# Kernel tuning notes

Hardware: AMD Instinct MI355X
Metric: run time of the kernel (lower is better)

Reference implementation:

```python
import jax, jax.numpy as jnp
import numpy as np

H = 128
L = 3
N = 100000
E = 1600000
G = 1024
OUT = 10
MAX_LEVEL = 1000
MAX_THOUGHTS = 5000
N_CATE = 5
BN_EPS = 1e-5


def _make_pe(n_pos, h):
    pos = np.arange(n_pos, dtype=np.float32)[:, None]
    div = np.exp(np.arange(0, h, 2, dtype=np.float32) * (-np.log(10000.0) / h))
    pe = np.zeros((n_pos, h), dtype=np.float32)
    pe[:, 0::2] = np.sin(pos * div)
    pe[:, 1::2] = np.cos(pos * div)
    return jnp.asarray(pe)


def setup_inputs() -> dict:
    key = jax.random.key(0)
    ks = jax.random.split(key, 16)
    s = 0.02
    inp = {
        "x": jax.random.randint(ks[0], (N, 3), 0, 5, dtype=jnp.int64 if jax.config.jax_enable_x64 else jnp.int32),
        "edge_index": jax.random.randint(ks[1], (2, E), 0, N),
        "batch": jnp.sort(jax.random.randint(ks[2], (N,), 0, G)),
        "num_graphs": G,
        "pe": _make_pe(MAX_THOUGHTS, H),
        "cate_emb": jax.random.normal(ks[3], (N_CATE, H), jnp.float32) * s,
        "level_emb": jax.random.normal(ks[4], (MAX_LEVEL, H), jnp.float32) * s,
        "conv_W1": jax.random.normal(ks[5], (L, H, H), jnp.float32) * s,
        "conv_b1": jnp.zeros((L, H), jnp.float32),
        "conv_g1": jnp.ones((L, H), jnp.float32),
        "conv_be1": jnp.zeros((L, H), jnp.float32),
        "conv_W2": jax.random.normal(ks[6], (L, H, H), jnp.float32) * s,
        "conv_b2": jnp.zeros((L, H), jnp.float32),
        "norm_g": jnp.ones((L, H), jnp.float32),
        "norm_be": jnp.zeros((L, H), jnp.float32),
        "gate_W1": jax.random.normal(ks[7], (H, H), jnp.float32) * s,
        "gate_b1": jnp.zeros((H,), jnp.float32),
        "gate_W2": jax.random.normal(ks[8], (H, 1), jnp.float32) * s,
        "gate_b2": jnp.zeros((1,), jnp.float32),
        "cls_W1": jax.random.normal(ks[9], (H, H), jnp.float32) * s,
        "cls_b1": jnp.zeros((H,), jnp.float32),
        "cls_g": jnp.ones((H,), jnp.float32),
        "cls_be": jnp.zeros((H,), jnp.float32),
        "cls_W2": jax.random.normal(ks[10], (H, OUT), jnp.float32) * s,
        "cls_b2": jnp.zeros((OUT,), jnp.float32),
    }
    return inp


def _bn(h, g, b):
    # BatchNorm1d, training mode: batch stats over the node/graph dim, biased var
    m = jnp.mean(h, axis=0)
    v = jnp.var(h, axis=0)
    return (h - m) * jax.lax.rsqrt(v + BN_EPS) * g + b


def reference(x, edge_index, batch, num_graphs, pe, cate_emb, level_emb,
              conv_W1, conv_b1, conv_g1, conv_be1, conv_W2, conv_b2,
              norm_g, norm_be, gate_W1, gate_b1, gate_W2, gate_b2,
              cls_W1, cls_b1, cls_g, cls_be, cls_W2, cls_b2):
    # NodeEncoder ('tree'): level + cate + sinusoidal thought PE
    level = jnp.clip(x[:, 0], 0, MAX_LEVEL - 1)
    cate = jnp.clip(x[:, 1], 0, N_CATE - 1)
    thought = jnp.clip(x[:, 2], 0, MAX_THOUGHTS - 1)
    h = cate_emb[cate] + level_emb[level] + pe[thought]  # [N, H]

    src, dst = edge_index[0], edge_index[1]
    n = h.shape[0]
    for i in range(L):
        # GINConv (eps=0): h_i <- MLP(h_i + sum_{j->i} h_j)
        agg = jax.ops.segment_sum(h[src], dst, num_segments=n)
        z = (h + agg) @ conv_W1[i] + conv_b1[i]
        z = jax.nn.relu(_bn(z, conv_g1[i], conv_be1[i]))
        z = z @ conv_W2[i] + conv_b2[i]
        h = jax.nn.relu(_bn(z, norm_g[i], norm_be[i]))

    # GlobalAttention pooling: per-graph softmax over gate scores
    gate = (jax.nn.relu(h @ gate_W1 + gate_b1) @ gate_W2 + gate_b2)[:, 0]  # [N]
    m = jax.ops.segment_max(gate, batch, num_segments=num_graphs)
    e = jnp.exp(gate - m[batch])
    s = jax.ops.segment_sum(e, batch, num_segments=num_graphs)
    alpha = e / s[batch]
    pooled = jax.ops.segment_sum(alpha[:, None] * h, batch, num_segments=num_graphs)  # [G, H]

    # classifier (dropout = 0)
    z = pooled @ cls_W1 + cls_b1
    z = jax.nn.relu(_bn(z, cls_g, cls_be))
    return z @ cls_W2 + cls_b2  # [G, OUT]
```

## Files before the change

### kernel.cpp

```cpp
#include <hip/hip_runtime.h>
#include <math.h>

#define HD 128

typedef __attribute__((ext_vector_type(8))) short bf16x8;
typedef __attribute__((ext_vector_type(8))) unsigned short us8;
typedef __attribute__((ext_vector_type(4))) unsigned short us4;
typedef __attribute__((ext_vector_type(4))) float f32x4;

__device__ __forceinline__ float bf2f(unsigned short u) {
  union { unsigned int i; float f; } v; v.i = ((unsigned int)u) << 16; return v.f;
}
__device__ __forceinline__ unsigned short f2bf(float f) {
  union { float f; unsigned int i; } v; v.f = f;
  unsigned int u = v.i;
  u += 0x7FFFu + ((u >> 16) & 1u);
  return (unsigned short)(u >> 16);
}

__global__ void zero_f(float* p, int n) {
  int i = blockIdx.x * blockDim.x + threadIdx.x;
  if (i < n) p[i] = 0.f;
}

__global__ void zero_int(int* p, int n) {
  int stride = gridDim.x * blockDim.x;
  for (int i = blockIdx.x * blockDim.x + threadIdx.x; i < n; i += stride) p[i] = 0;
}

__global__ void encode_kernel(const int* __restrict__ x, const float* __restrict__ pe,
                              const float* __restrict__ ce, const float* __restrict__ le,
                              float* __restrict__ h, int n) {
  int total = n * HD;
  int stride = gridDim.x * blockDim.x;
  for (int idx = blockIdx.x * blockDim.x + threadIdx.x; idx < total; idx += stride) {
    int node = idx >> 7, c = idx & (HD - 1);
    int lv = x[node * 3 + 0]; lv = lv < 0 ? 0 : (lv > 999 ? 999 : lv);
    int ct = x[node * 3 + 1]; ct = ct < 0 ? 0 : (ct > 4 ? 4 : ct);
    int th = x[node * 3 + 2]; th = th < 0 ? 0 : (th > 4999 ? 4999 : th);
    h[idx] = ce[ct * HD + c] + le[lv * HD + c] + pe[th * HD + c];
  }
}

__global__ void prep_w(const float* __restrict__ cW1, const float* __restrict__ cW2,
                       const float* __restrict__ gW1,
                       unsigned short* __restrict__ whi, unsigned short* __restrict__ wlo) {
  int m = blockIdx.x;
  const float* W = (m < 3) ? cW1 + (size_t)m * HD * HD
                 : (m < 6) ? cW2 + (size_t)(m - 3) * HD * HD : gW1;
  unsigned short* oh = whi + (size_t)m * HD * HD;
  unsigned short* ol = wlo + (size_t)m * HD * HD;
  for (int i = threadIdx.x; i < HD * HD; i += 256) {
    int j = i & 7;
    int l = (i >> 3) & 63;
    int p = i >> 9;
    int ct = p >> 2, k4 = p & 3;
    int c = ct * 16 + (l & 15);
    int k = (k4 * 4 + (l >> 4)) * 8 + j;
    float f = W[k * HD + c];
    unsigned short hh = f2bf(f);
    oh[i] = hh;
    ol[i] = f2bf(f - bf2f(hh));
  }
}


__global__ void hist_kernel(const int* __restrict__ ei, int* deg, int E, int Wwin) {
  int pass = blockIdx.x & 7;
  int b = blockIdx.x >> 3;
  int tstride = (gridDim.x >> 3) * blockDim.x;
  for (int e = b * blockDim.x + threadIdx.x; e < E; e += tstride) {
    int d = ei[E + e];
    if (d / Wwin == pass) atomicAdd(&deg[d], 1);
  }
}

#define SCAN_BS 1024
__global__ void scan1_kernel(const int* __restrict__ deg, int* __restrict__ off,
                             int* __restrict__ bsum, int n) {
  __shared__ int sh[256];
  int b = blockIdx.x, t = threadIdx.x;
  int base = b * SCAN_BS + t * 4;
  int v[4];
#pragma unroll
  for (int j = 0; j < 4; j++) v[j] = (base + j < n) ? deg[base + j] : 0;
  int s = v[0] + v[1] + v[2] + v[3];
  sh[t] = s;
  __syncthreads();
  for (int o = 1; o < 256; o <<= 1) {
    int x = (t >= o) ? sh[t - o] : 0;
    __syncthreads();
    sh[t] += x;
    __syncthreads();
  }
  int excl = sh[t] - s;
  if (t == 255) bsum[b] = sh[255];
  int run = excl;
#pragma unroll
  for (int j = 0; j < 4; j++) {
    if (base + j < n) off[base + j] = run;
    run += v[j];
  }
}

__global__ void scan2_kernel(int* bsum, int nb) {
  __shared__ int sh[128];
  int t = threadIdx.x;
  int v = (t < nb) ? bsum[t] : 0;
  sh[t] = v;
  __syncthreads();
  for (int o = 1; o < 128; o <<= 1) {
    int x = (t >= o) ? sh[t - o] : 0;
    __syncthreads();
    sh[t] += x;
    __syncthreads();
  }
  if (t < nb) bsum[t] = sh[t] - v;
}

__global__ void scan3_kernel(int* off, int* cursor, const int* __restrict__ bsum,
                             int n, int E) {
  int idx = blockIdx.x * blockDim.x + threadIdx.x;
  int stride = gridDim.x * blockDim.x;
  for (int i = idx; i < n; i += stride) {
    int v = off[i] + bsum[i >> 10];
    off[i] = v;
    cursor[i] = v;
  }
  if (idx == 0) off[n] = E;
}

__global__ void fill_kernel(const int* __restrict__ ei, int* cursor, int* csr_src,
                            int E, int Wwin) {
  int pass = blockIdx.x & 7;
  int b = blockIdx.x >> 3;
  int tstride = (gridDim.x >> 3) * blockDim.x;
  for (int e = b * blockDim.x + threadIdx.x; e < E; e += tstride) {
    int d = ei[E + e];
    if (d / Wwin == pass) {
      int pos = atomicAdd(&cursor[d], 1);
      csr_src[pos] = ei[e];
    }
  }
}

template<bool BN, bool STATS>
__global__ __launch_bounds__(512, 4)
void gemm_gather(const float* __restrict__ h, const int* __restrict__ off,
                 const int* __restrict__ src, const float* __restrict__ ab,
                 const unsigned short* __restrict__ Whi,
                 const unsigned short* __restrict__ Wlo,
                 const float* __restrict__ bias, float* __restrict__ outf,
                 float* __restrict__ stat, int Nn) {
  __shared__ unsigned short XsH[128 * HD];
  __shared__ unsigned short XsL[128 * HD];
  __shared__ float red[2 * HD];
  int t = threadIdx.x;
  long rowbase = (long)blockIdx.x * 128;
  int grp = t >> 5, lane = t & 31;

  float4 a4, b4;
  if (BN) {
    a4 = *(const float4*)(ab + lane * 4);
    b4 = *(const float4*)(ab + HD + lane * 4);
  }
#define APPLY_BN(v) if (BN) { \
    v.x = fmaxf(v.x * a4.x + b4.x, 0.f); \
    v.y = fmaxf(v.y * a4.y + b4.y, 0.f); \
    v.z = fmaxf(v.z * a4.z + b4.z, 0.f); \
    v.w = fmaxf(v.w * a4.w + b4.w, 0.f); }

  for (int rr = 0; rr < 8; rr++) {
    int r = grp + rr * 16;
    long row = rowbase + r; if (row > Nn - 1) row = Nn - 1;
    int s0 = off[row], s1 = off[row + 1];
    float4 acc0 = *(const float4*)(h + row * HD + lane * 4);
    APPLY_BN(acc0);
    float4 acc1 = {0.f, 0.f, 0.f, 0.f};
    float4 acc2 = {0.f, 0.f, 0.f, 0.f};
    float4 acc3 = {0.f, 0.f, 0.f, 0.f};
    int e = s0;
    for (; e + 8 <= s1; e += 8) {
      int i0 = src[e], i1 = src[e + 1], i2 = src[e + 2], i3 = src[e + 3];
      int i4 = src[e + 4], i5 = src[e + 5], i6 = src[e + 6], i7 = src[e + 7];
      float4 v0 = *(const float4*)(h + (size_t)i0 * HD + lane * 4);
      float4 v1 = *(const float4*)(h + (size_t)i1 * HD + lane * 4);
      float4 v2 = *(const float4*)(h + (size_t)i2 * HD + lane * 4);
      float4 v3 = *(const float4*)(h + (size_t)i3 * HD + lane * 4);
      float4 v4 = *(const float4*)(h + (size_t)i4 * HD + lane * 4);
      float4 v5 = *(const float4*)(h + (size_t)i5 * HD + lane * 4);
      float4 v6 = *(const float4*)(h + (size_t)i6 * HD + lane * 4);
      float4 v7 = *(const float4*)(h + (size_t)i7 * HD + lane * 4);
      APPLY_BN(v0); APPLY_BN(v1); APPLY_BN(v2); APPLY_BN(v3);
      APPLY_BN(v4); APPLY_BN(v5); APPLY_BN(v6); APPLY_BN(v7);
      acc0.x += v0.x + v4.x; acc0.y += v0.y + v4.y; acc0.z += v0.z + v4.z; acc0.w += v0.w + v4.w;
      acc1.x += v1.x + v5.x; acc1.y += v1.y + v5.y; acc1.z += v1.z + v5.z; acc1.w += v1.w + v5.w;
      acc2.x += v2.x + v6.x; acc2.y += v2.y + v6.y; acc2.z += v2.z + v6.z; acc2.w += v2.w + v6.w;
      acc3.x += v3.x + v7.x; acc3.y += v3.y + v7.y; acc3.z += v3.z + v7.z; acc3.w += v3.w + v7.w;
    }
    for (; e < s1; e++) {
      int s = src[e];
      float4 v = *(const float4*)(h + (size_t)s * HD + lane * 4);
      APPLY_BN(v);
      acc0.x += v.x; acc0.y += v.y; acc0.z += v.z; acc0.w += v.w;
    }
    acc0.x += acc1.x + acc2.x + acc3.x;
    acc0.y += acc1.y + acc2.y + acc3.y;
    acc0.z += acc1.z + acc2.z + acc3.z;
    acc0.w += acc1.w + acc2.w + acc3.w;
    float f[4] = {acc0.x, acc0.y, acc0.z, acc0.w};
    us4 hi, lo;
#pragma unroll
    for (int j = 0; j < 4; j++) {
      unsigned short hh = f2bf(f[j]);
      hi[j] = hh;
      lo[j] = f2bf(f[j] - bf2f(hh));
    }
    int g8 = lane >> 1;
    int offl = r * HD + (((g8 ^ (r & 7)) << 3)) + (lane & 1) * 4;
    *(us4*)(XsH + offl) = hi;
    *(us4*)(XsL + offl) = lo;
  }
#undef APPLY_BN
  if (STATS && t < 2 * HD) red[t] = 0.f;
  __syncthreads();

  int w = t >> 6, l = t & 63;
  int lr = l & 15, lg = l >> 4;

  f32x4 acc[8];
#pragma unroll
  for (int ct = 0; ct < 8; ct++) acc[ct] = (f32x4){0.f, 0.f, 0.f, 0.f};

  bf16x8 aH[4], aL[4];
  int arow = w * 16 + lr;
#pragma unroll
  for (int k4 = 0; k4 < 4; k4++) {
    int kg = k4 * 4 + lg;
    int offa = arow * HD + (((kg ^ (arow & 7)) << 3));
    aH[k4] = *(bf16x8*)(XsH + offa);
    aL[k4] = *(bf16x8*)(XsL + offa);
  }
#pragma unroll
  for (int ct = 0; ct < 8; ct++) {
#pragma unroll
    for (int k4 = 0; k4 < 4; k4++) {
      int bo = (((ct << 2) + k4) * 64 + l) * 8;
      bf16x8 bH = *(const bf16x8*)(Whi + bo);
      bf16x8 bL = *(const bf16x8*)(Wlo + bo);
      acc[ct] = __builtin_amdgcn_mfma_f32_16x16x32_bf16(aH[k4], bH, acc[ct], 0, 0, 0);
      acc[ct] = __builtin_amdgcn_mfma_f32_16x16x32_bf16(aH[k4], bL, acc[ct], 0, 0, 0);
      acc[ct] = __builtin_amdgcn_mfma_f32_16x16x32_bf16(aL[k4], bH, acc[ct], 0, 0, 0);
    }
  }

  float s[8], ss[8];
#pragma unroll
  for (int ct = 0; ct < 8; ct++) { s[ct] = 0.f; ss[ct] = 0.f; }
#pragma unroll
  for (int jj = 0; jj < 4; jj++) {
    long row = rowbase + w * 16 + lg * 4 + jj;
    bool ok = row < Nn;
#pragma unroll
    for (int ct = 0; ct < 8; ct++) {
      float v = acc[ct][jj] + bias[ct * 16 + lr];
      if (ok) {
        outf[row * HD + ct * 16 + lr] = v;
        if (STATS) { s[ct] += v; ss[ct] += v * v; }
      }
    }
  }
  if (STATS) {
#pragma unroll
    for (int ct = 0; ct < 8; ct++) {
      float sv = s[ct], sq = ss[ct];
      sv += __shfl_xor(sv, 16); sq += __shfl_xor(sq, 16);
      sv += __shfl_xor(sv, 32); sq += __shfl_xor(sq, 32);
      if (lg == 0) {
        atomicAdd(&red[ct * 16 + lr], sv);
        atomicAdd(&red[HD + ct * 16 + lr], sq);
      }
    }
    __syncthreads();
    float* st = stat + (blockIdx.x & 3) * 256;
    if (t < HD) {
      atomicAdd(&st[t], red[t]);
      atomicAdd(&st[HD + t], red[HD + t]);
    }
  }
}

template<bool INBN, bool GATE, bool STATS>
__global__ __launch_bounds__(512, 4)
void gemm_split(const float* __restrict__ X, const unsigned short* __restrict__ Whi,
                const unsigned short* __restrict__ Wlo,
                const float* __restrict__ bias, const float* __restrict__ ab,
                const float* __restrict__ w2, float* __restrict__ outf,
                float* __restrict__ gate, float* __restrict__ stat, int Nn) {
  __shared__ unsigned short XsH[128 * HD];
  __shared__ unsigned short XsL[128 * HD];
  __shared__ float red[2 * HD];
  int t = threadIdx.x;
  long rowbase = (long)blockIdx.x * 128;

#pragma unroll
  for (int it = 0; it < 8; it++) {
    int i = (t + it * 512) * 4;
    int r = i >> 7, k = i & (HD - 1);
    long row = rowbase + r; if (row > Nn - 1) row = Nn - 1;
    float4 v = *(const float4*)(X + row * HD + k);
    float f[4] = {v.x, v.y, v.z, v.w};
    if (INBN) {
#pragma unroll
      for (int j = 0; j < 4; j++)
        f[j] = fmaxf(f[j] * ab[k + j] + ab[HD + k + j], 0.f);
    }
    us4 hi, lo;
#pragma unroll
    for (int j = 0; j < 4; j++) {
      unsigned short hh = f2bf(f[j]);
      hi[j] = hh;
      lo[j] = f2bf(f[j] - bf2f(hh));
    }
    int g = k >> 3;
    int off = r * HD + ((((g ^ (r & 7)) << 3)) | (k & 7));
    *(us4*)(XsH + off) = hi;
    *(us4*)(XsL + off) = lo;
  }
  if (STATS && t < 2 * HD) red[t] = 0.f;
  __syncthreads();

  int w = t >> 6, l = t & 63;
  int lr = l & 15, lg = l >> 4;

  f32x4 acc[8];
#pragma unroll
  for (int ct = 0; ct < 8; ct++) acc[ct] = (f32x4){0.f, 0.f, 0.f, 0.f};

  bf16x8 aH[4], aL[4];
  int arow = w * 16 + lr;
#pragma unroll
  for (int k4 = 0; k4 < 4; k4++) {
    int kg = k4 * 4 + lg;
    int off = arow * HD + (((kg ^ (arow & 7)) << 3));
    aH[k4] = *(bf16x8*)(XsH + off);
    aL[k4] = *(bf16x8*)(XsL + off);
  }
#pragma unroll
  for (int ct = 0; ct < 8; ct++) {
#pragma unroll
    for (int k4 = 0; k4 < 4; k4++) {
      int bo = (((ct << 2) + k4) * 64 + l) * 8;
      bf16x8 bH = *(const bf16x8*)(Whi + bo);
      bf16x8 bL = *(const bf16x8*)(Wlo + bo);
      acc[ct] = __builtin_amdgcn_mfma_f32_16x16x32_bf16(aH[k4], bH, acc[ct], 0, 0, 0);
      acc[ct] = __builtin_amdgcn_mfma_f32_16x16x32_bf16(aH[k4], bL, acc[ct], 0, 0, 0);
      acc[ct] = __builtin_amdgcn_mfma_f32_16x16x32_bf16(aL[k4], bH, acc[ct], 0, 0, 0);
    }
  }

  if (GATE) {
#pragma unroll
    for (int jj = 0; jj < 4; jj++) {
      float p = 0.f;
#pragma unroll
      for (int ct = 0; ct < 8; ct++) {
        float v = fmaxf(acc[ct][jj] + bias[ct * 16 + lr], 0.f);
        p += v * w2[ct * 16 + lr];
      }
      p += __shfl_xor(p, 1);
      p += __shfl_xor(p, 2);
      p += __shfl_xor(p, 4);
      p += __shfl_xor(p, 8);
      long row = rowbase + w * 16 + lg * 4 + jj;
      if (lr == 0 && row < Nn) gate[row] = p;
    }
  } else {
    float s[8], ss[8];
#pragma unroll
    for (int ct = 0; ct < 8; ct++) { s[ct] = 0.f; ss[ct] = 0.f; }
#pragma unroll
    for (int jj = 0; jj < 4; jj++) {
      long row = rowbase + w * 16 + lg * 4 + jj;
      bool ok = row < Nn;
#pragma unroll
      for (int ct = 0; ct < 8; ct++) {
        float v = acc[ct][jj] + bias[ct * 16 + lr];
        if (ok) {
          outf[row * HD + ct * 16 + lr] = v;
          if (STATS) { s[ct] += v; ss[ct] += v * v; }
        }
      }
    }
    if (STATS) {
#pragma unroll
      for (int ct = 0; ct < 8; ct++) {
        float sv = s[ct], sq = ss[ct];
        sv += __shfl_xor(sv, 16); sq += __shfl_xor(sq, 16);
        sv += __shfl_xor(sv, 32); sq += __shfl_xor(sq, 32);
        if (lg == 0) {
          atomicAdd(&red[ct * 16 + lr], sv);
          atomicAdd(&red[HD + ct * 16 + lr], sq);
        }
      }
      __syncthreads();
      float* st = stat + (blockIdx.x & 3) * 256;
      if (t < HD) {
        atomicAdd(&st[t], red[t]);
        atomicAdd(&st[HD + t], red[HD + t]);
      }
    }
  }
}

__global__ void finalize_kernel(const float* __restrict__ stat, const float* __restrict__ g,
                                const float* __restrict__ be, float* ab, float inv_n) {
  int c = threadIdx.x;
  float s = stat[c] + stat[256 + c] + stat[512 + c] + stat[768 + c];
  float sq = stat[HD + c] + stat[256 + HD + c] + stat[512 + HD + c] + stat[768 + HD + c];
  float mean = s * inv_n;
  float var = sq * inv_n - mean * mean;
  float inv = rsqrtf(var + 1e-5f);
  float a = inv * g[c];
  ab[c] = a;
  ab[HD + c] = be[c] - mean * a;
}

__global__ void finalize1_kernel(const float* __restrict__ stat, const float* __restrict__ g,
                                 const float* __restrict__ be, float* ab, float inv_n) {
  int c = threadIdx.x;
  float mean = stat[c] * inv_n;
  float var = stat[HD + c] * inv_n - mean * mean;
  float inv = rsqrtf(var + 1e-5f);
  float a = inv * g[c];
  ab[c] = a;
  ab[HD + c] = be[c] - mean * a;
}

__global__ void bound_kernel(const int* __restrict__ batch, int* gs, int N, int G) {
  int i = blockIdx.x * blockDim.x + threadIdx.x;
  if (i >= N) return;
  int b = batch[i];
  int prev = (i == 0) ? -1 : batch[i - 1];
  for (int g = prev + 1; g <= b; g++) gs[g] = i;
  if (i == N - 1)
    for (int g = b + 1; g <= G; g++) gs[g] = N;
}

__global__ void fused_pool(const float* __restrict__ h, const float* __restrict__ gate,
                           const int* __restrict__ gs, const float* __restrict__ ab,
                           float* __restrict__ pooled) {
  int g = blockIdx.x;
  int t = threadIdx.x;
  int s0 = gs[g], s1 = gs[g + 1];
  if (s0 >= s1) { pooled[(size_t)g * HD + t] = 0.f; return; }
  __shared__ float red[HD];
  float m = -INFINITY;
  for (int i = s0 + t; i < s1; i += HD) m = fmaxf(m, gate[i]);
  red[t] = m;
  __syncthreads();
  for (int o = 64; o > 0; o >>= 1) {
    if (t < o) red[t] = fmaxf(red[t], red[t + o]);
    __syncthreads();
  }
  m = red[0];
  __syncthreads();
  float s = 0.f;
  for (int i = s0 + t; i < s1; i += HD) s += expf(gate[i] - m);
  red[t] = s;
  __syncthreads();
  for (int o = 64; o > 0; o >>= 1) {
    if (t < o) red[t] += red[t + o];
    __syncthreads();
  }
  float inv = 1.f / red[0];
  float a = ab[t], b = ab[HD + t];
  float acc = 0.f;
  int i = s0;
  for (; i + 4 <= s1; i += 4) {
    float al0 = expf(gate[i] - m);
    float al1 = expf(gate[i + 1] - m);
    float al2 = expf(gate[i + 2] - m);
    float al3 = expf(gate[i + 3] - m);
    float v0 = fmaxf(h[(size_t)(i + 0) * HD + t] * a + b, 0.f);
    float v1 = fmaxf(h[(size_t)(i + 1) * HD + t] * a + b, 0.f);
    float v2 = fmaxf(h[(size_t)(i + 2) * HD + t] * a + b, 0.f);
    float v3 = fmaxf(h[(size_t)(i + 3) * HD + t] * a + b, 0.f);
    acc += al0 * v0 + al1 * v1 + al2 * v2 + al3 * v3;
  }
  for (; i < s1; i++) {
    float al = expf(gate[i] - m);
    float v = fmaxf(h[(size_t)i * HD + t] * a + b, 0.f);
    acc += al * v;
  }
  pooled[(size_t)g * HD + t] = acc * inv;
}

__global__ __launch_bounds__(256, 4)
void gemm_f32(const float* __restrict__ X, const float* __restrict__ W,
              const float* __restrict__ bias, float* __restrict__ out, int Nn) {
  __shared__ float XsT[32][132];
  __shared__ float Ws[32][HD];
  int t = threadIdx.x;
  int r0 = (t >> 4) * 8;
  int c0 = (t & 15) * 8;
  long rowbase = (long)blockIdx.x * 128;

  float acc[8][8];
#pragma unroll
  for (int ci = 0; ci < 8; ci++) {
    float bv = bias[c0 + ci];
#pragma unroll
    for (int ri = 0; ri < 8; ri++) acc[ri][ci] = bv;
  }

  int sr = t >> 1;
  int hf = t & 1;
  long srow = rowbase + sr; if (srow > Nn - 1) srow = Nn - 1;
  const float* xrow = X + srow * HD;

  for (int k0 = 0; k0 < HD; k0 += 32) {
    __syncthreads();
#pragma unroll
    for (int j = 0; j < 4; j++) {
      int i = j * 1024 + t * 4;
      int kk = i >> 7, c = i & (HD - 1);
      *(float4*)&Ws[kk][c] = *(const float4*)&W[(size_t)(k0 + kk) * HD + c];
    }
#pragma unroll
    for (int j = 0; j < 4; j++) {
      int kc = k0 + hf * 16 + j * 4;
      float4 v = *(const float4*)&xrow[kc];
      int kl = hf * 16 + j * 4;
      XsT[kl + 0][sr] = v.x;
      XsT[kl + 1][sr] = v.y;
      XsT[kl + 2][sr] = v.z;
      XsT[kl + 3][sr] = v.w;
    }
    __syncthreads();
#pragma unroll 8
    for (int kk = 0; kk < 32; kk++) {
      float4 a0 = *(float4*)&XsT[kk][r0];
      float4 a1 = *(float4*)&XsT[kk][r0 + 4];
      float4 b0 = *(float4*)&Ws[kk][c0];
      float4 b1 = *(float4*)&Ws[kk][c0 + 4];
      float ar[8] = {a0.x, a0.y, a0.z, a0.w, a1.x, a1.y, a1.z, a1.w};
      float bc[8] = {b0.x, b0.y, b0.z, b0.w, b1.x, b1.y, b1.z, b1.w};
#pragma unroll
      for (int ri = 0; ri < 8; ri++)
#pragma unroll
        for (int ci = 0; ci < 8; ci++) acc[ri][ci] += ar[ri] * bc[ci];
    }
  }

#pragma unroll
  for (int ri = 0; ri < 8; ri++) {
    long row = rowbase + r0 + ri;
    if (row < Nn) {
      float4 o0 = {acc[ri][0], acc[ri][1], acc[ri][2], acc[ri][3]};
      float4 o1 = {acc[ri][4], acc[ri][5], acc[ri][6], acc[ri][7]};
      *(float4*)&out[row * HD + c0] = o0;
      *(float4*)&out[row * HD + c0 + 4] = o1;
    }
  }
}

__global__ void stats_f32(const float* __restrict__ z, float* stat, int n) {
  int c = threadIdx.x & (HD - 1);
  int rg = threadIdx.x >> 7;
  float s = 0.f, ss = 0.f;
  for (int r = blockIdx.x * 2 + rg; r < n; r += gridDim.x * 2) {
    float v = z[(size_t)r * HD + c];
    s += v; ss += v * v;
  }
  __shared__ float S[2][HD], SS[2][HD];
  S[rg][c] = s; SS[rg][c] = ss;
  __syncthreads();
  if (threadIdx.x < HD) {
    atomicAdd(&stat[c], S[0][c] + S[1][c]);
    atomicAdd(&stat[HD + c], SS[0][c] + SS[1][c]);
  }
}

__global__ void cls_out_kernel(const float* __restrict__ zc, const float* __restrict__ ab,
                               const float* __restrict__ W2, const float* __restrict__ b2,
                               float* out, int G) {
  int row = blockIdx.x;
  int t = threadIdx.x;
  float v0 = fmaxf(zc[(size_t)row * HD + t] * ab[t] + ab[HD + t], 0.f);
  float v1 = fmaxf(zc[(size_t)row * HD + 64 + t] * ab[64 + t] + ab[HD + 64 + t], 0.f);
  for (int o = 0; o < 10; o++) {
    float p = v0 * W2[t * 10 + o] + v1 * W2[(64 + t) * 10 + o];
#pragma unroll
    for (int s = 32; s > 0; s >>= 1) p += __shfl_down(p, s);
    if (t == 0) out[row * 10 + o] = p + b2[o];
  }
}

extern "C" void kernel_launch(void* const* d_in, const int* in_sizes, int n_in,
                              void* d_out, int out_size, void* d_ws, size_t ws_size,
                              hipStream_t stream) {
  const int* x     = (const int*)d_in[0];
  const int* ei    = (const int*)d_in[1];
  const int* batch = (const int*)d_in[2];
  const float* pe  = (const float*)d_in[4];
  const float* ce  = (const float*)d_in[5];
  const float* le  = (const float*)d_in[6];
  const float* cW1 = (const float*)d_in[7];
  const float* cb1 = (const float*)d_in[8];
  const float* cg1 = (const float*)d_in[9];
  const float* cbe1= (const float*)d_in[10];
  const float* cW2 = (const float*)d_in[11];
  const float* cb2 = (const float*)d_in[12];
  const float* ngm = (const float*)d_in[13];
  const float* nbe = (const float*)d_in[14];
  const float* gW1 = (const float*)d_in[15];
  const float* gb1 = (const float*)d_in[16];
  const float* gW2 = (const float*)d_in[17];
  const float* clW1= (const float*)d_in[19];
  const float* clb1= (const float*)d_in[20];
  const float* clg = (const float*)d_in[21];
  const float* clbe= (const float*)d_in[22];
  const float* clW2= (const float*)d_in[23];
  const float* clb2= (const float*)d_in[24];

  int N = in_sizes[2];
  int E = in_sizes[1] / 2;
  int G = out_size / 10;

  float* buf0   = (float*)d_ws;
  float* buf1   = buf0 + (size_t)N * HD;
  float* pooled = buf1 + (size_t)N * HD;
  float* gate   = pooled + (size_t)G * HD;
  float* zc     = gate + N;
  float* stats  = zc + (size_t)G * HD;
  float* ab     = stats + 7 * 1024;
  unsigned short* whi = (unsigned short*)(ab + 7 * 256);
  unsigned short* wlo = whi + 7 * HD * HD;
  int* csr_off  = (int*)(wlo + 7 * HD * HD);
  int* cursor   = csr_off + (N + 1);
  int* bsum     = cursor + N;
  int* gs       = bsum + 128;
  int* csr_src  = gs + (G + 1);

  float* out = (float*)d_out;
  int gemmBlocks = (N + 127) / 128;
  int Wwin = (N + 7) / 8;

  zero_f<<<28, 256, 0, stream>>>(stats, 7 * 1024);
  encode_kernel<<<2048, 256, 0, stream>>>(x, pe, ce, le, buf0, N);
  prep_w<<<7, 256, 0, stream>>>(cW1, cW2, gW1, whi, wlo);

  int nb = (N + SCAN_BS - 1) / SCAN_BS;
  zero_int<<<256, 256, 0, stream>>>(cursor, N);
  hist_kernel<<<2048, 256, 0, stream>>>(ei, cursor, E, Wwin);
  scan1_kernel<<<nb, 256, 0, stream>>>(cursor, csr_off, bsum, N);
  scan2_kernel<<<1, 128, 0, stream>>>(bsum, nb);
  scan3_kernel<<<256, 256, 0, stream>>>(csr_off, cursor, bsum, N, E);
  fill_kernel<<<2048, 256, 0, stream>>>(ei, cursor, csr_src, E, Wwin);
  bound_kernel<<<(N + 255) / 256, 256, 0, stream>>>(batch, gs, N, G);

  for (int l = 0; l < 3; l++) {
    float* abPrev = ab + (l - 1) * 512 + 256;
    if (l == 0)
      gemm_gather<false, true><<<gemmBlocks, 512, 0, stream>>>(
          buf0, csr_off, csr_src, nullptr,
          whi + (size_t)l * HD * HD, wlo + (size_t)l * HD * HD,
          cb1 + l * HD, buf1, stats + l * 2048, N);
    else
      gemm_gather<true, true><<<gemmBlocks, 512, 0, stream>>>(
          buf0, csr_off, csr_src, abPrev,
          whi + (size_t)l * HD * HD, wlo + (size_t)l * HD * HD,
          cb1 + l * HD, buf1, stats + l * 2048, N);
    finalize_kernel<<<1, 128, 0, stream>>>(stats + l * 2048, cg1 + l * HD, cbe1 + l * HD,
                                           ab + l * 512, 1.f / N);
    gemm_split<true, false, true><<<gemmBlocks, 512, 0, stream>>>(
        buf1, whi + (size_t)(3 + l) * HD * HD, wlo + (size_t)(3 + l) * HD * HD,
        cb2 + l * HD, ab + l * 512, nullptr, buf0, nullptr, stats + l * 2048 + 1024, N);
    finalize_kernel<<<1, 128, 0, stream>>>(stats + l * 2048 + 1024, ngm + l * HD, nbe + l * HD,
                                           ab + l * 512 + 256, 1.f / N);
  }

  const float* abFin = ab + 2 * 512 + 256;
  gemm_split<true, true, false><<<gemmBlocks, 512, 0, stream>>>(
      buf0, whi + (size_t)6 * HD * HD, wlo + (size_t)6 * HD * HD,
      gb1, abFin, gW2, nullptr, gate, nullptr, N);
  fused_pool<<<G, HD, 0, stream>>>(buf0, gate, gs, abFin, pooled);

  gemm_f32<<<(G + 127) / 128, 256, 0, stream>>>(pooled, clW1, clb1, zc, G);
  stats_f32<<<64, 256, 0, stream>>>(zc, stats + 6 * 1024, G);
  finalize1_kernel<<<1, 128, 0, stream>>>(stats + 6 * 1024, clg, clbe, ab + 6 * 256, 1.f / G);
  cls_out_kernel<<<G, 64, 0, stream>>>(zc, ab + 6 * 256, clW2, clb2, out, G);
}
```

Before: 890.6 us.

## Halve GEMM row tile to 64 and split columns across waves for occupancy

The gather-GEMM and split-GEMM kernels now process 64 rows per block instead of 128. The 8 waves are arranged as 4 row groups by 2 column halves, so each wave holds 4 accumulator tiles instead of 8. The launch-bounds occupancy hint rises from 4 to 8 blocks per CU, since LDS use and registers per block are halved. Gate outputs are now reduced across the two column halves through a shared-memory atomic. The cost is twice as many blocks, more global stat atomics, and each weight fragment being fetched by more blocks.

```diff
diff --git a/kernel.cpp b/kernel.cpp
--- a/kernel.cpp
+++ b/kernel.cpp
@@ -54,8 +54,8 @@
     int j = i & 7;
     int l = (i >> 3) & 63;
     int p = i >> 9;
-    int ct = p >> 2, k4 = p & 3;
-    int c = ct * 16 + (l & 15);
+    int cg = p >> 2, k4 = p & 3;
+    int c = cg * 16 + (l & 15);
     int k = (k4 * 4 + (l >> 4)) * 8 + j;
     float f = W[k * HD + c];
     unsigned short hh = f2bf(f);
@@ -145,18 +145,18 @@
 }
 
 template<bool BN, bool STATS>
-__global__ __launch_bounds__(512, 4)
+__global__ __launch_bounds__(512, 8)
 void gemm_gather(const float* __restrict__ h, const int* __restrict__ off,
                  const int* __restrict__ src, const float* __restrict__ ab,
                  const unsigned short* __restrict__ Whi,
                  const unsigned short* __restrict__ Wlo,
                  const float* __restrict__ bias, float* __restrict__ outf,
                  float* __restrict__ stat, int Nn) {
-  __shared__ unsigned short XsH[128 * HD];
-  __shared__ unsigned short XsL[128 * HD];
+  __shared__ unsigned short XsH[64 * HD];
+  __shared__ unsigned short XsL[64 * HD];
   __shared__ float red[2 * HD];
   int t = threadIdx.x;
-  long rowbase = (long)blockIdx.x * 128;
+  long rowbase = (long)blockIdx.x * 64;
   int grp = t >> 5, lane = t & 31;
 
   float4 a4, b4;
@@ -170,7 +170,7 @@
     v.z = fmaxf(v.z * a4.z + b4.z, 0.f); \
     v.w = fmaxf(v.w * a4.w + b4.w, 0.f); }
 
-  for (int rr = 0; rr < 8; rr++) {
+  for (int rr = 0; rr < 4; rr++) {
     int r = grp + rr * 16;
     long row = rowbase + r; if (row > Nn - 1) row = Nn - 1;
     int s0 = off[row], s1 = off[row + 1];
@@ -227,13 +227,14 @@
 
   int w = t >> 6, l = t & 63;
   int lr = l & 15, lg = l >> 4;
-
-  f32x4 acc[8];
-#pragma unroll
-  for (int ct = 0; ct < 8; ct++) acc[ct] = (f32x4){0.f, 0.f, 0.f, 0.f};
+  int wr = w & 3, wc = w >> 2;
+
+  f32x4 acc[4];
+#pragma unroll
+  for (int ct = 0; ct < 4; ct++) acc[ct] = (f32x4){0.f, 0.f, 0.f, 0.f};
 
   bf16x8 aH[4], aL[4];
-  int arow = w * 16 + lr;
+  int arow = wr * 16 + lr;
 #pragma unroll
   for (int k4 = 0; k4 < 4; k4++) {
     int kg = k4 * 4 + lg;
@@ -242,10 +243,11 @@
     aL[k4] = *(bf16x8*)(XsL + offa);
   }
 #pragma unroll
-  for (int ct = 0; ct < 8; ct++) {
+  for (int ct = 0; ct < 4; ct++) {
+    int cg = wc * 4 + ct;
 #pragma unroll
     for (int k4 = 0; k4 < 4; k4++) {
-      int bo = (((ct << 2) + k4) * 64 + l) * 8;
+      int bo = (((cg << 2) + k4) * 64 + l) * 8;
       bf16x8 bH = *(const bf16x8*)(Whi + bo);
       bf16x8 bL = *(const bf16x8*)(Wlo + bo);
       acc[ct] = __builtin_amdgcn_mfma_f32_16x16x32_bf16(aH[k4], bH, acc[ct], 0, 0, 0);
@@ -254,57 +256,57 @@
     }
   }
 
-  float s[8], ss[8];
-#pragma unroll
-  for (int ct = 0; ct < 8; ct++) { s[ct] = 0.f; ss[ct] = 0.f; }
+  float s[4], ss[4];
+#pragma unroll
+  for (int ct = 0; ct < 4; ct++) { s[ct] = 0.f; ss[ct] = 0.f; }
 #pragma unroll
   for (int jj = 0; jj < 4; jj++) {
-    long row = rowbase + w * 16 + lg * 4 + jj;
+    long row = rowbase + wr * 16 + lg * 4 + jj;
     bool ok = row < Nn;
 #pragma unroll
-    for (int ct = 0; ct < 8; ct++) {
-      float v = acc[ct][jj] + bias[ct * 16 + lr];
+    for (int ct = 0; ct < 4; ct++) {
+      int col = (wc * 4 + ct) * 16 + lr;
+      float v = acc[ct][jj] + bias[col];
       if (ok) {
-        outf[row * HD + ct * 16 + lr] = v;
+        outf[row * HD + col] = v;
         if (STATS) { s[ct] += v; ss[ct] += v * v; }
       }
     }
   }
   if (STATS) {
 #pragma unroll
-    for (int ct = 0; ct < 8; ct++) {
+    for (int ct = 0; ct < 4; ct++) {
+      int col = (wc * 4 + ct) * 16 + lr;
       float sv = s[ct], sq = ss[ct];
       sv += __shfl_xor(sv, 16); sq += __shfl_xor(sq, 16);
       sv += __shfl_xor(sv, 32); sq += __shfl_xor(sq, 32);
       if (lg == 0) {
-        atomicAdd(&red[ct * 16 + lr], sv);
-        atomicAdd(&red[HD + ct * 16 + lr], sq);
+        atomicAdd(&red[col], sv);
+        atomicAdd(&red[HD + col], sq);
       }
     }
     __syncthreads();
     float* st = stat + (blockIdx.x & 3) * 256;
-    if (t < HD) {
-      atomicAdd(&st[t], red[t]);
-      atomicAdd(&st[HD + t], red[HD + t]);
-    }
+    if (t < 2 * HD) atomicAdd(&st[t], red[t]);
   }
 }
 
 template<bool INBN, bool GATE, bool STATS>
-__global__ __launch_bounds__(512, 4)
+__global__ __launch_bounds__(512, 8)
 void gemm_split(const float* __restrict__ X, const unsigned short* __restrict__ Whi,
                 const unsigned short* __restrict__ Wlo,
                 const float* __restrict__ bias, const float* __restrict__ ab,
                 const float* __restrict__ w2, float* __restrict__ outf,
                 float* __restrict__ gate, float* __restrict__ stat, int Nn) {
-  __shared__ unsigned short XsH[128 * HD];
-  __shared__ unsigned short XsL[128 * HD];
+  __shared__ unsigned short XsH[64 * HD];
+  __shared__ unsigned short XsL[64 * HD];
   __shared__ float red[2 * HD];
+  __shared__ float gred[64];
   int t = threadIdx.x;
-  long rowbase = (long)blockIdx.x * 128;
-
-#pragma unroll
-  for (int it = 0; it < 8; it++) {
+  long rowbase = (long)blockIdx.x * 64;
+
+#pragma unroll
+  for (int it = 0; it < 4; it++) {
     int i = (t + it * 512) * 4;
     int r = i >> 7, k = i & (HD - 1);
     long row = rowbase + r; if (row > Nn - 1) row = Nn - 1;
@@ -328,17 +330,19 @@
     *(us4*)(XsL + off) = lo;
   }
   if (STATS && t < 2 * HD) red[t] = 0.f;
+  if (GATE && t < 64) gred[t] = 0.f;
   __syncthreads();
 
   int w = t >> 6, l = t & 63;
   int lr = l & 15, lg = l >> 4;
-
-  f32x4 acc[8];
-#pragma unroll
-  for (int ct = 0; ct < 8; ct++) acc[ct] = (f32x4){0.f, 0.f, 0.f, 0.f};
+  int wr = w & 3, wc = w >> 2;
+
+  f32x4 acc[4];
+#pragma unroll
+  for (int ct = 0; ct < 4; ct++) acc[ct] = (f32x4){0.f, 0.f, 0.f, 0.f};
 
   bf16x8 aH[4], aL[4];
-  int arow = w * 16 + lr;
+  int arow = wr * 16 + lr;
 #pragma unroll
   for (int k4 = 0; k4 < 4; k4++) {
     int kg = k4 * 4 + lg;
@@ -347,10 +351,11 @@
     aL[k4] = *(bf16x8*)(XsL + off);
   }
 #pragma unroll
-  for (int ct = 0; ct < 8; ct++) {
+  for (int ct = 0; ct < 4; ct++) {
+    int cg = wc * 4 + ct;
 #pragma unroll
     for (int k4 = 0; k4 < 4; k4++) {
-      int bo = (((ct << 2) + k4) * 64 + l) * 8;
+      int bo = (((cg << 2) + k4) * 64 + l) * 8;
       bf16x8 bH = *(const bf16x8*)(Whi + bo);
       bf16x8 bL = *(const bf16x8*)(Wlo + bo);
       acc[ct] = __builtin_amdgcn_mfma_f32_16x16x32_bf16(aH[k4], bH, acc[ct], 0, 0, 0);
@@ -364,51 +369,52 @@
     for (int jj = 0; jj < 4; jj++) {
       float p = 0.f;
 #pragma unroll
-      for (int ct = 0; ct < 8; ct++) {
-        float v = fmaxf(acc[ct][jj] + bias[ct * 16 + lr], 0.f);
-        p += v * w2[ct * 16 + lr];
+      for (int ct = 0; ct < 4; ct++) {
+        int col = (wc * 4 + ct) * 16 + lr;
+        float v = fmaxf(acc[ct][jj] + bias[col], 0.f);
+        p += v * w2[col];
       }
       p += __shfl_xor(p, 1);
       p += __shfl_xor(p, 2);
       p += __shfl_xor(p, 4);
       p += __shfl_xor(p, 8);
-      long row = rowbase + w * 16 + lg * 4 + jj;
-      if (lr == 0 && row < Nn) gate[row] = p;
-    }
+      if (lr == 0) atomicAdd(&gred[wr * 16 + lg * 4 + jj], p);
+    }
+    __syncthreads();
+    if (t < 64 && rowbase + t < Nn) gate[rowbase + t] = gred[t];
   } else {
-    float s[8], ss[8];
-#pragma unroll
-    for (int ct = 0; ct < 8; ct++) { s[ct] = 0.f; ss[ct] = 0.f; }
+    float s[4], ss[4];
+#pragma unroll
+    for (int ct = 0; ct < 4; ct++) { s[ct] = 0.f; ss[ct] = 0.f; }
 #pragma unroll
     for (int jj = 0; jj < 4; jj++) {
-      long row = rowbase + w * 16 + lg * 4 + jj;
+      long row = rowbase + wr * 16 + lg * 4 + jj;
       bool ok = row < Nn;
 #pragma unroll
-      for (int ct = 0; ct < 8; ct++) {
-        float v = acc[ct][jj] + bias[ct * 16 + lr];
+      for (int ct = 0; ct < 4; ct++) {
+        int col = (wc * 4 + ct) * 16 + lr;
+        float v = acc[ct][jj] + bias[col];
         if (ok) {
-          outf[row * HD + ct * 16 + lr] = v;
+          outf[row * HD + col] = v;
           if (STATS) { s[ct] += v; ss[ct] += v * v; }
         }
       }
     }
     if (STATS) {
 #pragma unroll
-      for (int ct = 0; ct < 8; ct++) {
+      for (int ct = 0; ct < 4; ct++) {
+        int col = (wc * 4 + ct) * 16 + lr;
         float sv = s[ct], sq = ss[ct];
         sv += __shfl_xor(sv, 16); sq += __shfl_xor(sq, 16);
         sv += __shfl_xor(sv, 32); sq += __shfl_xor(sq, 32);
         if (lg == 0) {
-          atomicAdd(&red[ct * 16 + lr], sv);
-          atomicAdd(&red[HD + ct * 16 + lr], sq);
+          atomicAdd(&red[col], sv);
+          atomicAdd(&red[HD + col], sq);
         }
       }
       __syncthreads();
       float* st = stat + (blockIdx.x & 3) * 256;
-      if (t < HD) {
-        atomicAdd(&st[t], red[t]);
-        atomicAdd(&st[HD + t], red[HD + t]);
-      }
+      if (t < 2 * HD) atomicAdd(&st[t], red[t]);
     }
   }
 }
@@ -644,7 +650,7 @@
   int* csr_src  = gs + (G + 1);
 
   float* out = (float*)d_out;
-  int gemmBlocks = (N + 127) / 128;
+  int gemmBlocks = (N + 63) / 64;
   int Wwin = (N + 7) / 8;
 
   zero_f<<<28, 256, 0, stream>>>(stats, 7 * 1024);
```

New measurement: 926.9 us. +4.1%, slower.
